# Kernel tuning notes

Measured on AMD Instinct MI355X. Metric: run time of the kernel, lower is better.

The kernel has to match this reference:

```python
import jax, jax.numpy as jnp
import numpy as np

LN_EPS = 1e-5


def _layer_norm(x, g, b):
    m = jnp.mean(x, axis=-1, keepdims=True)
    v = jnp.mean(jnp.square(x - m), axis=-1, keepdims=True)
    return (x - m) * jax.lax.rsqrt(v + LN_EPS) * g + b


def _transition(x, g, bln, w_sw, w_ss, w_sig, b_sig, w_scale, residual):
    # TransitionBlock, eval mode (dropout = identity)
    x_in = x
    x = _layer_norm(x, g, bln)
    b = jax.nn.silu(x @ w_sw.T) * (x @ w_ss.T)
    y = jax.nn.sigmoid(x @ w_sig.T + b_sig) * (b @ w_scale.T)
    return x_in + y if residual else y


def setup_inputs() -> dict:
    N, E = 1000000, 100000
    F_DIM, A_DIM, H_DIM, HEADS = 64, 128, 256, 4
    D_IN = F_DIM + A_DIM
    key = jax.random.key(0)
    ks = jax.random.split(key, 16)
    s = 0.02
    inp = {
        'v_equivariant': jax.random.normal(ks[0], (N, 3), jnp.float32),
        'v_atom_features': jax.random.normal(ks[1], (N, A_DIM), jnp.float32),
        'edge_group_idx': jnp.sort(jax.random.randint(ks[2], (N,), 0, E)).astype(jnp.int32),
        'num_edges': E,
        'fourier_w': jax.random.normal(ks[3], (F_DIM,), jnp.float32),
        'fourier_b': jax.random.normal(ks[4], (F_DIM,), jnp.float32),
        # TransitionBlock 1 (input 192 -> 256, no residual)
        'tb1_ln_g': jnp.ones((D_IN,), jnp.float32),
        'tb1_ln_b': jnp.zeros((D_IN,), jnp.float32),
        'tb1_w_sw': jax.random.normal(ks[5], (H_DIM, D_IN), jnp.float32) * s,
        'tb1_w_ss': jax.random.normal(ks[6], (H_DIM, D_IN), jnp.float32) * s,
        'tb1_w_sig': jax.random.normal(ks[7], (H_DIM, D_IN), jnp.float32) * s,
        'tb1_b_sig': jnp.full((H_DIM,), -2.0, jnp.float32),
        'tb1_w_scale': jax.random.normal(ks[8], (H_DIM, H_DIM), jnp.float32) * s,
        # TransitionBlock 2 (256 -> 256, residual)
        'tb2_ln_g': jnp.ones((H_DIM,), jnp.float32),
        'tb2_ln_b': jnp.zeros((H_DIM,), jnp.float32),
        'tb2_w_sw': jax.random.normal(ks[9], (H_DIM, H_DIM), jnp.float32) * s,
        'tb2_w_ss': jax.random.normal(ks[10], (H_DIM, H_DIM), jnp.float32) * s,
        'tb2_w_sig': jax.random.normal(ks[11], (H_DIM, H_DIM), jnp.float32) * s,
        'tb2_b_sig': jnp.full((H_DIM,), -2.0, jnp.float32),
        'tb2_w_scale': jax.random.normal(ks[12], (H_DIM, H_DIM), jnp.float32) * s,
        # final linear 256 -> num_heads
        'out_w': jax.random.normal(ks[13], (HEADS, H_DIM), jnp.float32) * s,
        'out_b': jnp.zeros((HEADS,), jnp.float32),
    }
    return inp


def reference(v_equivariant, v_atom_features, edge_group_idx, num_edges,
              fourier_w, fourier_b,
              tb1_ln_g, tb1_ln_b, tb1_w_sw, tb1_w_ss, tb1_w_sig, tb1_b_sig, tb1_w_scale,
              tb2_ln_g, tb2_ln_b, tb2_w_sw, tb2_w_ss, tb2_w_sig, tb2_b_sig, tb2_w_scale,
              out_w, out_b):
    # Fourier embedding of vector norms: [N] -> [N, F_DIM]
    v_norms = jnp.linalg.norm(v_equivariant, axis=-1)
    f_dist = jnp.cos(2.0 * jnp.pi * (v_norms[..., None] * fourier_w + fourier_b))
    x = jnp.concatenate([f_dist, v_atom_features], axis=-1)  # [N, 192]
    x = _transition(x, tb1_ln_g, tb1_ln_b, tb1_w_sw, tb1_w_ss, tb1_w_sig, tb1_b_sig, tb1_w_scale, residual=False)
    x = _transition(x, tb2_ln_g, tb2_ln_b, tb2_w_sw, tb2_w_ss, tb2_w_sig, tb2_b_sig, tb2_w_scale, residual=True)
    scores = x @ out_w.T + out_b  # [N, H]
    # scatter_softmax over edge groups (per head)
    smax = jax.ops.segment_max(scores, edge_group_idx, num_segments=num_edges)
    e = jnp.exp(scores - smax[edge_group_idx])
    ssum = jax.ops.segment_sum(e, edge_group_idx, num_segments=num_edges)
    alphas = e / ssum[edge_group_idx]  # [N, H]
    # weighted scatter-sum pooling of 3-vectors per head
    v_weighted = v_equivariant[:, None, :] * alphas[..., None]  # [N, H, 3]
    v_pooled = jax.ops.segment_sum(v_weighted, edge_group_idx, num_segments=num_edges)
    return v_pooled.reshape(num_edges, -1)  # [E, H*3]
```

## Files before the change

kernel.cpp:

```cpp
#include <hip/hip_runtime.h>
#include <math.h>

#define DIN   192
#define HD    256
#define ROWS  64
#define THREADS 256
#define LSTR  256

typedef __bf16 bf16_t;
typedef bf16_t bf16x8 __attribute__((ext_vector_type(8)));
typedef unsigned short u16x8 __attribute__((ext_vector_type(8)));
typedef float  f32x16 __attribute__((ext_vector_type(16)));

static __device__ __forceinline__ f32x16 mfma32(bf16x8 a, bf16x8 b, f32x16 c) {
  return __builtin_amdgcn_mfma_f32_32x32x16_bf16(a, b, c, 0, 0, 0);
}
static __device__ __forceinline__ unsigned short f2bfu(float f) {
  bf16_t h = (bf16_t)f; unsigned short u; __builtin_memcpy(&u, &h, 2); return u;
}
static __device__ __forceinline__ float bfu2f(unsigned short u) {
  unsigned x = ((unsigned)u) << 16; float f; __builtin_memcpy(&f, &x, 4); return f;
}
static __device__ __forceinline__ unsigned pk2(float a, float b) {
  return (unsigned)f2bfu(a) | ((unsigned)f2bfu(b) << 16);
}
static __device__ __forceinline__ float lo16(unsigned u) { return bfu2f((unsigned short)(u & 0xffff)); }
static __device__ __forceinline__ float hi16(unsigned u) { return bfu2f((unsigned short)(u >> 16)); }
static __device__ __forceinline__ float sigm(float x) {
  return __builtin_amdgcn_rcpf(1.f + __expf(-x));
}
static __device__ __forceinline__ int lidx(int row, int col) {
  return row * LSTR + (col ^ ((row & 7) << 3));
}
static __device__ __forceinline__ int crow(int r, int kg) {
  return (r & 3) + 8 * (r >> 2) + 4 * kg;
}

#define OFF_WSW1 0
#define OFF_WSS1 49152
#define OFF_WSG1 98304
#define OFF_WSC1 147456
#define OFF_WSW2 212992
#define OFF_WSS2 278528
#define OFF_WSG2 344064
#define OFF_WSC2 409600
#define OFF_WOUT 475136
#define NGRP_REORD 59392
#define NGRP_ALL   60416

__global__ void iab_wconv_kernel(const float* __restrict__ a0, const float* __restrict__ a1,
                                 const float* __restrict__ a2, const float* __restrict__ a3,
                                 const float* __restrict__ a4, const float* __restrict__ a5,
                                 const float* __restrict__ a6, const float* __restrict__ a7,
                                 const float* __restrict__ a8, unsigned short* __restrict__ out)
{
  const int i = blockIdx.x * 256 + threadIdx.x;
  if (i >= NGRP_ALL) return;
  if (i >= NGRP_REORD) {
    const int g  = i - NGRP_REORD;
    const int ks = g >> 6;
    const int ln = g & 63;
    const int col = ln & 31;
    const int kg  = ln >> 5;
    #pragma unroll
    for (int j = 0; j < 8; ++j) {
      const float vv = (col < 4) ? a8[col * 256 + ks * 16 + kg * 8 + j] : 0.f;
      out[OFF_WOUT + (size_t)g * 8 + j] = f2bfu(vv);
    }
    return;
  }
  const float* src; int off, Kd, g;
  if      (i < 6144)  { src = a0; off = OFF_WSW1; Kd = 192; g = i; }
  else if (i < 12288) { src = a1; off = OFF_WSS1; Kd = 192; g = i - 6144; }
  else if (i < 18432) { src = a2; off = OFF_WSG1; Kd = 192; g = i - 12288; }
  else if (i < 26624) { src = a3; off = OFF_WSC1; Kd = 256; g = i - 18432; }
  else if (i < 34816) { src = a4; off = OFF_WSW2; Kd = 256; g = i - 26624; }
  else if (i < 43008) { src = a5; off = OFF_WSS2; Kd = 256; g = i - 34816; }
  else if (i < 51200) { src = a6; off = OFF_WSG2; Kd = 256; g = i - 43008; }
  else                { src = a7; off = OFF_WSC2; Kd = 256; g = i - 51200; }
  const int KS   = Kd >> 4;
  const int tile = g / (KS * 64);
  const int rem  = g - tile * (KS * 64);
  const int ks   = rem >> 6;
  const int ln   = rem & 63;
  const float* sp = src + (size_t)(tile * 32 + (ln & 31)) * Kd + ks * 16 + (ln >> 5) * 8;
  #pragma unroll
  for (int j = 0; j < 8; ++j) out[off + (size_t)g * 8 + j] = f2bfu(sp[j]);
}

template<int KS>
static __device__ __forceinline__ void bphase2(const unsigned short* __restrict__ Wsw,
                                               const unsigned short* __restrict__ Wss,
                                               const unsigned short* __restrict__ sIn,
                                               unsigned short* __restrict__ sOut,
                                               int l31, int kg, int xr, int ocol)
{
  f32x16 u0{}, u1{}, s0{}, s1{};
  #pragma unroll 2
  for (int ks = 0; ks < KS; ++ks) {
    const bf16x8 wa = *(const bf16x8*)(Wsw + ks * 512);
    const bf16x8 wb = *(const bf16x8*)(Wss + ks * 512);
    const int off = ((ks * 16) + kg * 8) ^ xr;
    const bf16x8 A0 = *(const bf16x8*)(sIn + l31 * LSTR + off);
    const bf16x8 A1 = *(const bf16x8*)(sIn + (32 + l31) * LSTR + off);
    u0 = mfma32(A0, wa, u0); u1 = mfma32(A1, wa, u1);
    s0 = mfma32(A0, wb, s0); s1 = mfma32(A1, wb, s1);
  }
  #pragma unroll
  for (int i = 0; i < 16; ++i) {
    const float x0 = u0[i];
    const float x1 = u1[i];
    sOut[lidx(crow(i, kg),      ocol)] = f2bfu(x0 * sigm(x0) * s0[i]);
    sOut[lidx(32 + crow(i, kg), ocol)] = f2bfu(x1 * sigm(x1) * s1[i]);
  }
}

template<int KSG, int RES>
static __device__ __forceinline__ void cphase2(const unsigned short* __restrict__ Wg,
                                               const unsigned short* __restrict__ Wc,
                                               const unsigned short* __restrict__ sAin,
                                               const unsigned short* __restrict__ sBin,
                                               int l31, int kg, int xr, float bias,
                                               unsigned (&x0)[8], unsigned (&x1)[8])
{
  unsigned pg0[8], pg1[8];
  {
    f32x16 g0{}, g1{};
    #pragma unroll 4
    for (int ks = 0; ks < KSG; ++ks) {
      const bf16x8 wg = *(const bf16x8*)(Wg + ks * 512);
      const int off = ((ks * 16) + kg * 8) ^ xr;
      const bf16x8 A0 = *(const bf16x8*)(sAin + l31 * LSTR + off);
      const bf16x8 A1 = *(const bf16x8*)(sAin + (32 + l31) * LSTR + off);
      g0 = mfma32(A0, wg, g0);
      g1 = mfma32(A1, wg, g1);
    }
    #pragma unroll
    for (int p = 0; p < 8; ++p) {
      pg0[p] = pk2(sigm(g0[2*p] + bias), sigm(g0[2*p+1] + bias));
      pg1[p] = pk2(sigm(g1[2*p] + bias), sigm(g1[2*p+1] + bias));
    }
  }
  {
    f32x16 c0{}, c1{};
    #pragma unroll 4
    for (int ks = 0; ks < 16; ++ks) {
      const bf16x8 wv = *(const bf16x8*)(Wc + ks * 512);
      const int off = ((ks * 16) + kg * 8) ^ xr;
      const bf16x8 A0 = *(const bf16x8*)(sBin + l31 * LSTR + off);
      const bf16x8 A1 = *(const bf16x8*)(sBin + (32 + l31) * LSTR + off);
      c0 = mfma32(A0, wv, c0);
      c1 = mfma32(A1, wv, c1);
    }
    #pragma unroll
    for (int p = 0; p < 8; ++p) {
      const float ya0 = lo16(pg0[p]) * c0[2*p],  ya1 = hi16(pg0[p]) * c0[2*p+1];
      const float yb0 = lo16(pg1[p]) * c1[2*p],  yb1 = hi16(pg1[p]) * c1[2*p+1];
      if (RES) {
        x0[p] = pk2(lo16(x0[p]) + ya0, hi16(x0[p]) + ya1);
        x1[p] = pk2(lo16(x1[p]) + yb0, hi16(x1[p]) + yb1);
      } else {
        x0[p] = pk2(ya0, ya1);
        x1[p] = pk2(yb0, yb1);
      }
    }
  }
}

static __device__ __forceinline__ void storePk2(unsigned short* dst,
                                                const unsigned (&x0)[8], const unsigned (&x1)[8],
                                                int kg, int ocol)
{
  #pragma unroll
  for (int p = 0; p < 8; ++p) {
    const int r0 = crow(2 * p, kg);
    dst[lidx(r0,          ocol)] = (unsigned short)(x0[p] & 0xffff);
    dst[lidx(r0 + 1,      ocol)] = (unsigned short)(x0[p] >> 16);
    dst[lidx(32 + r0,     ocol)] = (unsigned short)(x1[p] & 0xffff);
    dst[lidx(32 + r0 + 1, ocol)] = (unsigned short)(x1[p] >> 16);
  }
}

#define LNACC(P) { \
  float e_; \
  e_ = bfu2f(P[0]); s += e_; sq += e_ * e_; \
  e_ = bfu2f(P[1]); s += e_; sq += e_ * e_; \
  e_ = bfu2f(P[2]); s += e_; sq += e_ * e_; \
  e_ = bfu2f(P[3]); s += e_; sq += e_ * e_; \
  e_ = bfu2f(P[4]); s += e_; sq += e_ * e_; \
  e_ = bfu2f(P[5]); s += e_; sq += e_ * e_; \
  e_ = bfu2f(P[6]); s += e_; sq += e_ * e_; \
  e_ = bfu2f(P[7]); s += e_; sq += e_ * e_; }

#define LNNORM(P, GPTR, BPTR, BASE) { \
  const int base_ = (BASE); \
  const float4 ga_ = *(const float4*)((GPTR) + base_); \
  const float4 gb_ = *(const float4*)((GPTR) + base_ + 4); \
  const float4 oa_ = *(const float4*)((BPTR) + base_); \
  const float4 ob_ = *(const float4*)((BPTR) + base_ + 4); \
  u16x8 q_; \
  q_[0] = f2bfu((bfu2f(P[0]) - mean) * rstd * ga_.x + oa_.x); \
  q_[1] = f2bfu((bfu2f(P[1]) - mean) * rstd * ga_.y + oa_.y); \
  q_[2] = f2bfu((bfu2f(P[2]) - mean) * rstd * ga_.z + oa_.z); \
  q_[3] = f2bfu((bfu2f(P[3]) - mean) * rstd * ga_.w + oa_.w); \
  q_[4] = f2bfu((bfu2f(P[4]) - mean) * rstd * gb_.x + ob_.x); \
  q_[5] = f2bfu((bfu2f(P[5]) - mean) * rstd * gb_.y + ob_.y); \
  q_[6] = f2bfu((bfu2f(P[6]) - mean) * rstd * gb_.z + ob_.z); \
  q_[7] = f2bfu((bfu2f(P[7]) - mean) * rstd * gb_.w + ob_.w); \
  *(u16x8*)(sA + r * LSTR + (base_ ^ xrr)) = q_; }

__global__ __launch_bounds__(THREADS, 2)
void iab_rows_mfma(
    const float* __restrict__ v, const float* __restrict__ af,
    const float* __restrict__ fw, const float* __restrict__ fb,
    const float* __restrict__ ln1g, const float* __restrict__ ln1b,
    const float* __restrict__ bsig1,
    const float* __restrict__ ln2g, const float* __restrict__ ln2b,
    const float* __restrict__ bsig2,
    const float* __restrict__ outb,
    const unsigned short* __restrict__ wc,
    float* __restrict__ scores, int N)
{
  __shared__ __align__(16) unsigned short sA[ROWS * LSTR];
  __shared__ __align__(16) unsigned short sB[ROWS * LSTR];

  const int t    = threadIdx.x;
  const int w    = t >> 6;
  const int lane = t & 63;
  const int l31  = lane & 31;
  const int kg   = lane >> 5;
  const int xr   = (lane & 7) << 3;
  const int row0 = blockIdx.x * ROWS;
  const int oc0  = w * 64 + l31;
  const int oc1  = oc0 + 32;
  const int T0   = w * 2;
  const int T1   = w * 2 + 1;
  const int lb   = lane * 8;

  #pragma unroll 1
  for (int it = 0; it < 2; ++it) {
    const int r   = (t >> 3) + it * 32;
    const int sub = t & 7;
    const int g   = row0 + r;
    const int xrr = (r & 7) << 3;
    float s = 0.f, sq = 0.f;
    u16x8 p0, p1 = {}, p2 = {};
    {
      float vx = 0.f, vy = 0.f, vz = 0.f;
      if (g < N) {
        vx = v[3 * (size_t)g + 0];
        vy = v[3 * (size_t)g + 1];
        vz = v[3 * (size_t)g + 2];
      }
      const float nrm = sqrtf(vx * vx + vy * vy + vz * vz);
      const float4 fwa = *(const float4*)(fw + sub * 8);
      const float4 fwb = *(const float4*)(fw + sub * 8 + 4);
      const float4 fba = *(const float4*)(fb + sub * 8);
      const float4 fbb = *(const float4*)(fb + sub * 8 + 4);
      const float e0 = __cosf(6.283185307179586f * (nrm * fwa.x + fba.x));
      const float e1 = __cosf(6.283185307179586f * (nrm * fwa.y + fba.y));
      const float e2 = __cosf(6.283185307179586f * (nrm * fwa.z + fba.z));
      const float e3 = __cosf(6.283185307179586f * (nrm * fwa.w + fba.w));
      const float e4 = __cosf(6.283185307179586f * (nrm * fwb.x + fbb.x));
      const float e5 = __cosf(6.283185307179586f * (nrm * fwb.y + fbb.y));
      const float e6 = __cosf(6.283185307179586f * (nrm * fwb.z + fbb.z));
      const float e7 = __cosf(6.283185307179586f * (nrm * fwb.w + fbb.w));
      s  += e0 + e1 + e2 + e3 + e4 + e5 + e6 + e7;
      sq += e0*e0 + e1*e1 + e2*e2 + e3*e3 + e4*e4 + e5*e5 + e6*e6 + e7*e7;
      p0[0] = f2bfu(e0); p0[1] = f2bfu(e1); p0[2] = f2bfu(e2); p0[3] = f2bfu(e3);
      p0[4] = f2bfu(e4); p0[5] = f2bfu(e5); p0[6] = f2bfu(e6); p0[7] = f2bfu(e7);
    }
    if (g < N) {
      const float* ap = af + (size_t)g * 128 + sub * 8;
      {
        const float4 a0 = *(const float4*)(ap);
        const float4 a1 = *(const float4*)(ap + 4);
        s  += a0.x + a0.y + a0.z + a0.w + a1.x + a1.y + a1.z + a1.w;
        sq += a0.x*a0.x + a0.y*a0.y + a0.z*a0.z + a0.w*a0.w
            + a1.x*a1.x + a1.y*a1.y + a1.z*a1.z + a1.w*a1.w;
        p1[0] = f2bfu(a0.x); p1[1] = f2bfu(a0.y); p1[2] = f2bfu(a0.z); p1[3] = f2bfu(a0.w);
        p1[4] = f2bfu(a1.x); p1[5] = f2bfu(a1.y); p1[6] = f2bfu(a1.z); p1[7] = f2bfu(a1.w);
      }
      {
        const float4 a2 = *(const float4*)(ap + 64);
        const float4 a3 = *(const float4*)(ap + 68);
        s  += a2.x + a2.y + a2.z + a2.w + a3.x + a3.y + a3.z + a3.w;
        sq += a2.x*a2.x + a2.y*a2.y + a2.z*a2.z + a2.w*a2.w
            + a3.x*a3.x + a3.y*a3.y + a3.z*a3.z + a3.w*a3.w;
        p2[0] = f2bfu(a2.x); p2[1] = f2bfu(a2.y); p2[2] = f2bfu(a2.z); p2[3] = f2bfu(a2.w);
        p2[4] = f2bfu(a3.x); p2[5] = f2bfu(a3.y); p2[6] = f2bfu(a3.z); p2[7] = f2bfu(a3.w);
      }
    }
    #pragma unroll
    for (int o = 1; o < 8; o <<= 1) {
      s  += __shfl_xor(s,  o);
      sq += __shfl_xor(sq, o);
    }
    const float mean = s * (1.f / 192.f);
    const float var  = fmaxf(sq * (1.f / 192.f) - mean * mean, 0.f);
    const float rstd = rsqrtf(var + 1e-5f);
    LNNORM(p0, ln1g, ln1b, sub * 8);
    LNNORM(p1, ln1g, ln1b, 64 + sub * 8);
    LNNORM(p2, ln1g, ln1b, 128 + sub * 8);
  }
  __syncthreads();

  unsigned xT0M0[8], xT0M1[8], xT1M0[8], xT1M1[8];

  bphase2<12>(wc + OFF_WSW1 + T0 * 12 * 512 + lb,
              wc + OFF_WSS1 + T0 * 12 * 512 + lb, sA, sB, l31, kg, xr, oc0);
  __builtin_amdgcn_sched_barrier(0);
  bphase2<12>(wc + OFF_WSW1 + T1 * 12 * 512 + lb,
              wc + OFF_WSS1 + T1 * 12 * 512 + lb, sA, sB, l31, kg, xr, oc1);
  __syncthreads();

  cphase2<12, 0>(wc + OFF_WSG1 + T0 * 12 * 512 + lb,
                 wc + OFF_WSC1 + T0 * 16 * 512 + lb,
                 sA, sB, l31, kg, xr, bsig1[oc0], xT0M0, xT0M1);
  __builtin_amdgcn_sched_barrier(0);
  cphase2<12, 0>(wc + OFF_WSG1 + T1 * 12 * 512 + lb,
                 wc + OFF_WSC1 + T1 * 16 * 512 + lb,
                 sA, sB, l31, kg, xr, bsig1[oc1], xT1M0, xT1M1);
  __syncthreads();

  storePk2(sA, xT0M0, xT0M1, kg, oc0);
  storePk2(sA, xT1M0, xT1M1, kg, oc1);
  __syncthreads();

  #pragma unroll 1
  for (int it = 0; it < 2; ++it) {
    const int r   = (t >> 3) + it * 32;
    const int sub = t & 7;
    const int xrr = (r & 7) << 3;
    const u16x8 rv0 = *(const u16x8*)(sA + r * LSTR + ((sub * 32 +  0) ^ xrr));
    const u16x8 rv1 = *(const u16x8*)(sA + r * LSTR + ((sub * 32 +  8) ^ xrr));
    const u16x8 rv2 = *(const u16x8*)(sA + r * LSTR + ((sub * 32 + 16) ^ xrr));
    const u16x8 rv3 = *(const u16x8*)(sA + r * LSTR + ((sub * 32 + 24) ^ xrr));
    float s = 0.f, sq = 0.f;
    LNACC(rv0);
    LNACC(rv1);
    LNACC(rv2);
    LNACC(rv3);
    #pragma unroll
    for (int o = 1; o < 8; o <<= 1) {
      s  += __shfl_xor(s,  o);
      sq += __shfl_xor(sq, o);
    }
    const float mean = s * (1.f / 256.f);
    const float var  = fmaxf(sq * (1.f / 256.f) - mean * mean, 0.f);
    const float rstd = rsqrtf(var + 1e-5f);
    LNNORM(rv0, ln2g, ln2b, sub * 32 +  0);
    LNNORM(rv1, ln2g, ln2b, sub * 32 +  8);
    LNNORM(rv2, ln2g, ln2b, sub * 32 + 16);
    LNNORM(rv3, ln2g, ln2b, sub * 32 + 24);
  }
  __syncthreads();

  bphase2<16>(wc + OFF_WSW2 + T0 * 16 * 512 + lb,
              wc + OFF_WSS2 + T0 * 16 * 512 + lb, sA, sB, l31, kg, xr, oc0);
  __builtin_amdgcn_sched_barrier(0);
  bphase2<16>(wc + OFF_WSW2 + T1 * 16 * 512 + lb,
              wc + OFF_WSS2 + T1 * 16 * 512 + lb, sA, sB, l31, kg, xr, oc1);
  __syncthreads();

  cphase2<16, 1>(wc + OFF_WSG2 + T0 * 16 * 512 + lb,
                 wc + OFF_WSC2 + T0 * 16 * 512 + lb,
                 sA, sB, l31, kg, xr, bsig2[oc0], xT0M0, xT0M1);
  __builtin_amdgcn_sched_barrier(0);
  cphase2<16, 1>(wc + OFF_WSG2 + T1 * 16 * 512 + lb,
                 wc + OFF_WSC2 + T1 * 16 * 512 + lb,
                 sA, sB, l31, kg, xr, bsig2[oc1], xT1M0, xT1M1);
  __syncthreads();

  storePk2(sA, xT0M0, xT0M1, kg, oc0);
  storePk2(sA, xT1M0, xT1M1, kg, oc1);
  __syncthreads();

  if (w < 2) {
    const unsigned short* WtF = wc + OFF_WOUT + (size_t)lane * 8;
    f32x16 c{};
    #pragma unroll 4
    for (int ks = 0; ks < 16; ++ks) {
      const bf16x8 wf = *(const bf16x8*)(WtF + ks * 512);
      const bf16x8 A  = *(const bf16x8*)(sA + (w * 32 + l31) * LSTR + (((ks * 16) + kg * 8) ^ xr));
      c = mfma32(A, wf, c);
    }
    if (l31 < 4) {
      const float bias = outb[l31];
      #pragma unroll
      for (int i = 0; i < 16; ++i) {
        const int g = row0 + w * 32 + crow(i, kg);
        if (g < N) scores[(size_t)g * 4 + l31] = c[i] + bias;
      }
    }
  }
}

__device__ __forceinline__ int iab_lower_bound(const int* __restrict__ a, int n, int key)
{
  int lo = 0, hi = n;
  while (lo < hi) {
    const int mid = (lo + hi) >> 1;
    if (a[mid] < key) lo = mid + 1; else hi = mid;
  }
  return lo;
}

__global__ __launch_bounds__(256)
void iab_segpool_kernel(const float* __restrict__ scores,
                        const float* __restrict__ v,
                        const int* __restrict__ gidx,
                        float* __restrict__ out, int N, int E)
{
  const int seg  = blockIdx.x * 4 + (threadIdx.x >> 6);
  const int lane = threadIdx.x & 63;
  if (seg >= E) return;

  const int lo = iab_lower_bound(gidx, N, seg);
  const int hi = iab_lower_bound(gidx, N, seg + 1);

  const int h  = lane & 3;
  const int ro = lane >> 2;

  float m = -INFINITY;
  for (int base = lo; base < hi; base += 16) {
    const int r = base + ro;
    if (r < hi) m = fmaxf(m, scores[(size_t)r * 4 + h]);
  }
  #pragma unroll
  for (int o = 4; o < 64; o <<= 1) m = fmaxf(m, __shfl_xor(m, o));

  float ssum = 0.f, w0 = 0.f, w1 = 0.f, w2 = 0.f;
  for (int base = lo; base < hi; base += 16) {
    const int r = base + ro;
    if (r < hi) {
      const float e = expf(scores[(size_t)r * 4 + h] - m);
      ssum += e;
      w0 += e * v[3 * (size_t)r + 0];
      w1 += e * v[3 * (size_t)r + 1];
      w2 += e * v[3 * (size_t)r + 2];
    }
  }
  #pragma unroll
  for (int o = 4; o < 64; o <<= 1) {
    ssum += __shfl_xor(ssum, o);
    w0   += __shfl_xor(w0, o);
    w1   += __shfl_xor(w1, o);
    w2   += __shfl_xor(w2, o);
  }

  if (ro == 0) {
    const float inv = (hi > lo) ? (1.f / ssum) : 0.f;
    out[(size_t)seg * 12 + h * 3 + 0] = w0 * inv;
    out[(size_t)seg * 12 + h * 3 + 1] = w1 * inv;
    out[(size_t)seg * 12 + h * 3 + 2] = w2 * inv;
  }
}

extern "C" void kernel_launch(void* const* d_in, const int* in_sizes, int n_in,
                              void* d_out, int out_size, void* d_ws, size_t ws_size,
                              hipStream_t stream)
{
  const float* v     = (const float*)d_in[0];
  const float* af    = (const float*)d_in[1];
  const int*   gidx  = (const int*)  d_in[2];
  const float* fw    = (const float*)d_in[4];
  const float* fb    = (const float*)d_in[5];
  const float* ln1g  = (const float*)d_in[6];
  const float* ln1b  = (const float*)d_in[7];
  const float* wsw1  = (const float*)d_in[8];
  const float* wss1  = (const float*)d_in[9];
  const float* wsig1 = (const float*)d_in[10];
  const float* bsig1 = (const float*)d_in[11];
  const float* wsc1  = (const float*)d_in[12];
  const float* ln2g  = (const float*)d_in[13];
  const float* ln2b  = (const float*)d_in[14];
  const float* wsw2  = (const float*)d_in[15];
  const float* wss2  = (const float*)d_in[16];
  const float* wsig2 = (const float*)d_in[17];
  const float* bsig2 = (const float*)d_in[18];
  const float* wsc2  = (const float*)d_in[19];
  const float* outw  = (const float*)d_in[20];
  const float* outb  = (const float*)d_in[21];

  const int N = in_sizes[0] / 3;
  const int E = out_size / 12;

  float* scores = (float*)d_ws;
  unsigned short* wcv = (unsigned short*)((char*)d_ws + (size_t)N * 4 * sizeof(float));

  hipLaunchKernelGGL(iab_wconv_kernel, dim3((NGRP_ALL + 255) / 256), dim3(256), 0, stream,
                     wsw1, wss1, wsig1, wsc1, wsw2, wss2, wsig2, wsc2, outw, wcv);

  hipLaunchKernelGGL(iab_rows_mfma, dim3((N + ROWS - 1) / ROWS), dim3(THREADS), 0, stream,
                     v, af, fw, fb, ln1g, ln1b, bsig1, ln2g, ln2b, bsig2, outb,
                     wcv, scores, N);

  hipLaunchKernelGGL(iab_segpool_kernel, dim3((E + 3) / 4), dim3(256), 0, stream,
                     scores, v, gidx, (float*)d_out, N, E);
}
```

Baseline: 2.080 ms.

## Switch row kernel to 16x16x32 MFMA with 32-row tiles and higher occupancy

Result: slower. 2.433 ms (+17.0%).

```diff
diff --git a/kernel.cpp b/kernel.cpp
--- a/kernel.cpp
+++ b/kernel.cpp
@@ -3,17 +3,17 @@
 
 #define DIN   192
 #define HD    256
-#define ROWS  64
+#define ROWS  32
 #define THREADS 256
 #define LSTR  256
 
 typedef __bf16 bf16_t;
 typedef bf16_t bf16x8 __attribute__((ext_vector_type(8)));
 typedef unsigned short u16x8 __attribute__((ext_vector_type(8)));
-typedef float  f32x16 __attribute__((ext_vector_type(16)));
-
-static __device__ __forceinline__ f32x16 mfma32(bf16x8 a, bf16x8 b, f32x16 c) {
-  return __builtin_amdgcn_mfma_f32_32x32x16_bf16(a, b, c, 0, 0, 0);
+typedef float  f32x4  __attribute__((ext_vector_type(4)));
+
+static __device__ __forceinline__ f32x4 mfma16(bf16x8 a, bf16x8 b, f32x4 c) {
+  return __builtin_amdgcn_mfma_f32_16x16x32_bf16(a, b, c, 0, 0, 0);
 }
 static __device__ __forceinline__ unsigned short f2bfu(float f) {
   bf16_t h = (bf16_t)f; unsigned short u; __builtin_memcpy(&u, &h, 2); return u;
@@ -31,9 +31,6 @@
 }
 static __device__ __forceinline__ int lidx(int row, int col) {
   return row * LSTR + (col ^ ((row & 7) << 3));
-}
-static __device__ __forceinline__ int crow(int r, int kg) {
-  return (r & 3) + 8 * (r >> 2) + 4 * kg;
 }
 
 #define OFF_WSW1 0
@@ -46,7 +43,7 @@
 #define OFF_WSC2 409600
 #define OFF_WOUT 475136
 #define NGRP_REORD 59392
-#define NGRP_ALL   60416
+#define NGRP_ALL   59904
 
 __global__ void iab_wconv_kernel(const float* __restrict__ a0, const float* __restrict__ a1,
                                  const float* __restrict__ a2, const float* __restrict__ a3,
@@ -60,11 +57,11 @@
     const int g  = i - NGRP_REORD;
     const int ks = g >> 6;
     const int ln = g & 63;
-    const int col = ln & 31;
-    const int kg  = ln >> 5;
+    const int col = ln & 15;
+    const int g4  = ln >> 4;
     #pragma unroll
     for (int j = 0; j < 8; ++j) {
-      const float vv = (col < 4) ? a8[col * 256 + ks * 16 + kg * 8 + j] : 0.f;
+      const float vv = (col < 4) ? a8[col * 256 + ks * 32 + g4 * 8 + j] : 0.f;
       out[OFF_WOUT + (size_t)g * 8 + j] = f2bfu(vv);
     }
     return;
@@ -78,106 +75,105 @@
   else if (i < 43008) { src = a5; off = OFF_WSS2; Kd = 256; g = i - 34816; }
   else if (i < 51200) { src = a6; off = OFF_WSG2; Kd = 256; g = i - 43008; }
   else                { src = a7; off = OFF_WSC2; Kd = 256; g = i - 51200; }
-  const int KS   = Kd >> 4;
-  const int tile = g / (KS * 64);
-  const int rem  = g - tile * (KS * 64);
+  const int KS32 = Kd >> 5;
+  const int tile = g / (KS32 * 64);
+  const int rem  = g - tile * (KS32 * 64);
   const int ks   = rem >> 6;
   const int ln   = rem & 63;
-  const float* sp = src + (size_t)(tile * 32 + (ln & 31)) * Kd + ks * 16 + (ln >> 5) * 8;
+  const float* sp = src + (size_t)(tile * 16 + (ln & 15)) * Kd + ks * 32 + (ln >> 4) * 8;
   #pragma unroll
   for (int j = 0; j < 8; ++j) out[off + (size_t)g * 8 + j] = f2bfu(sp[j]);
 }
 
-template<int KS>
-static __device__ __forceinline__ void bphase2(const unsigned short* __restrict__ Wsw,
-                                               const unsigned short* __restrict__ Wss,
-                                               const unsigned short* __restrict__ sIn,
-                                               unsigned short* __restrict__ sOut,
-                                               int l31, int kg, int xr, int ocol)
-{
-  f32x16 u0{}, u1{}, s0{}, s1{};
+template<int KS32>
+static __device__ __forceinline__ void bphase16(const unsigned short* __restrict__ Wsw,
+                                                const unsigned short* __restrict__ Wss,
+                                                const unsigned short* __restrict__ sIn,
+                                                unsigned short* __restrict__ sOut,
+                                                int cc, int kb, int xr, int g4, int ocol)
+{
+  f32x4 u0{}, u1{}, s0{}, s1{};
   #pragma unroll 2
-  for (int ks = 0; ks < KS; ++ks) {
+  for (int ks = 0; ks < KS32; ++ks) {
     const bf16x8 wa = *(const bf16x8*)(Wsw + ks * 512);
     const bf16x8 wb = *(const bf16x8*)(Wss + ks * 512);
-    const int off = ((ks * 16) + kg * 8) ^ xr;
-    const bf16x8 A0 = *(const bf16x8*)(sIn + l31 * LSTR + off);
-    const bf16x8 A1 = *(const bf16x8*)(sIn + (32 + l31) * LSTR + off);
-    u0 = mfma32(A0, wa, u0); u1 = mfma32(A1, wa, u1);
-    s0 = mfma32(A0, wb, s0); s1 = mfma32(A1, wb, s1);
-  }
-  #pragma unroll
-  for (int i = 0; i < 16; ++i) {
-    const float x0 = u0[i];
-    const float x1 = u1[i];
-    sOut[lidx(crow(i, kg),      ocol)] = f2bfu(x0 * sigm(x0) * s0[i]);
-    sOut[lidx(32 + crow(i, kg), ocol)] = f2bfu(x1 * sigm(x1) * s1[i]);
-  }
-}
-
-template<int KSG, int RES>
-static __device__ __forceinline__ void cphase2(const unsigned short* __restrict__ Wg,
-                                               const unsigned short* __restrict__ Wc,
-                                               const unsigned short* __restrict__ sAin,
-                                               const unsigned short* __restrict__ sBin,
-                                               int l31, int kg, int xr, float bias,
-                                               unsigned (&x0)[8], unsigned (&x1)[8])
-{
-  unsigned pg0[8], pg1[8];
+    const int off = (ks * 32 + kb) ^ xr;
+    const bf16x8 A0 = *(const bf16x8*)(sIn + cc * LSTR + off);
+    const bf16x8 A1 = *(const bf16x8*)(sIn + (16 + cc) * LSTR + off);
+    u0 = mfma16(A0, wa, u0); u1 = mfma16(A1, wa, u1);
+    s0 = mfma16(A0, wb, s0); s1 = mfma16(A1, wb, s1);
+  }
+  #pragma unroll
+  for (int r = 0; r < 4; ++r) {
+    const float x0 = u0[r];
+    const float x1 = u1[r];
+    sOut[lidx(g4 * 4 + r,      ocol)] = f2bfu(x0 * sigm(x0) * s0[r]);
+    sOut[lidx(16 + g4 * 4 + r, ocol)] = f2bfu(x1 * sigm(x1) * s1[r]);
+  }
+}
+
+template<int KSG32, int RES>
+static __device__ __forceinline__ void cphase16(const unsigned short* __restrict__ Wg,
+                                                const unsigned short* __restrict__ Wc,
+                                                const unsigned short* __restrict__ sAin,
+                                                const unsigned short* __restrict__ sBin,
+                                                int cc, int kb, int xr, float bias,
+                                                unsigned (&x)[4])
+{
+  unsigned pg[4];
   {
-    f32x16 g0{}, g1{};
+    f32x4 g0{}, g1{};
     #pragma unroll 4
-    for (int ks = 0; ks < KSG; ++ks) {
+    for (int ks = 0; ks < KSG32; ++ks) {
       const bf16x8 wg = *(const bf16x8*)(Wg + ks * 512);
-      const int off = ((ks * 16) + kg * 8) ^ xr;
-      const bf16x8 A0 = *(const bf16x8*)(sAin + l31 * LSTR + off);
-      const bf16x8 A1 = *(const bf16x8*)(sAin + (32 + l31) * LSTR + off);
-      g0 = mfma32(A0, wg, g0);
-      g1 = mfma32(A1, wg, g1);
-    }
+      const int off = (ks * 32 + kb) ^ xr;
+      const bf16x8 A0 = *(const bf16x8*)(sAin + cc * LSTR + off);
+      const bf16x8 A1 = *(const bf16x8*)(sAin + (16 + cc) * LSTR + off);
+      g0 = mfma16(A0, wg, g0);
+      g1 = mfma16(A1, wg, g1);
+    }
+    pg[0] = pk2(sigm(g0[0] + bias), sigm(g0[1] + bias));
+    pg[1] = pk2(sigm(g0[2] + bias), sigm(g0[3] + bias));
+    pg[2] = pk2(sigm(g1[0] + bias), sigm(g1[1] + bias));
+    pg[3] = pk2(sigm(g1[2] + bias), sigm(g1[3] + bias));
+  }
+  {
+    f32x4 c0{}, c1{};
+    #pragma unroll 4
+    for (int ks = 0; ks < 8; ++ks) {
+      const bf16x8 wv = *(const bf16x8*)(Wc + ks * 512);
+      const int off = (ks * 32 + kb) ^ xr;
+      const bf16x8 A0 = *(const bf16x8*)(sBin + cc * LSTR + off);
+      const bf16x8 A1 = *(const bf16x8*)(sBin + (16 + cc) * LSTR + off);
+      c0 = mfma16(A0, wv, c0);
+      c1 = mfma16(A1, wv, c1);
+    }
+    if (RES) {
+      x[0] = pk2(lo16(x[0]) + lo16(pg[0]) * c0[0], hi16(x[0]) + hi16(pg[0]) * c0[1]);
+      x[1] = pk2(lo16(x[1]) + lo16(pg[1]) * c0[2], hi16(x[1]) + hi16(pg[1]) * c0[3]);
+      x[2] = pk2(lo16(x[2]) + lo16(pg[2]) * c1[0], hi16(x[2]) + hi16(pg[2]) * c1[1]);
+      x[3] = pk2(lo16(x[3]) + lo16(pg[3]) * c1[2], hi16(x[3]) + hi16(pg[3]) * c1[3]);
+    } else {
+      x[0] = pk2(lo16(pg[0]) * c0[0], hi16(pg[0]) * c0[1]);
+      x[1] = pk2(lo16(pg[1]) * c0[2], hi16(pg[1]) * c0[3]);
+      x[2] = pk2(lo16(pg[2]) * c1[0], hi16(pg[2]) * c1[1]);
+      x[3] = pk2(lo16(pg[3]) * c1[2], hi16(pg[3]) * c1[3]);
+    }
+  }
+}
+
+static __device__ __forceinline__ void storePk16(unsigned short* dst, const unsigned (&x)[4],
+                                                 int g4, int ocol)
+{
+  #pragma unroll
+  for (int m = 0; m < 2; ++m) {
     #pragma unroll
-    for (int p = 0; p < 8; ++p) {
-      pg0[p] = pk2(sigm(g0[2*p] + bias), sigm(g0[2*p+1] + bias));
-      pg1[p] = pk2(sigm(g1[2*p] + bias), sigm(g1[2*p+1] + bias));
-    }
-  }
-  {
-    f32x16 c0{}, c1{};
-    #pragma unroll 4
-    for (int ks = 0; ks < 16; ++ks) {
-      const bf16x8 wv = *(const bf16x8*)(Wc + ks * 512);
-      const int off = ((ks * 16) + kg * 8) ^ xr;
-      const bf16x8 A0 = *(const bf16x8*)(sBin + l31 * LSTR + off);
-      const bf16x8 A1 = *(const bf16x8*)(sBin + (32 + l31) * LSTR + off);
-      c0 = mfma32(A0, wv, c0);
-      c1 = mfma32(A1, wv, c1);
-    }
-    #pragma unroll
-    for (int p = 0; p < 8; ++p) {
-      const float ya0 = lo16(pg0[p]) * c0[2*p],  ya1 = hi16(pg0[p]) * c0[2*p+1];
-      const float yb0 = lo16(pg1[p]) * c1[2*p],  yb1 = hi16(pg1[p]) * c1[2*p+1];
-      if (RES) {
-        x0[p] = pk2(lo16(x0[p]) + ya0, hi16(x0[p]) + ya1);
-        x1[p] = pk2(lo16(x1[p]) + yb0, hi16(x1[p]) + yb1);
-      } else {
-        x0[p] = pk2(ya0, ya1);
-        x1[p] = pk2(yb0, yb1);
-      }
-    }
-  }
-}
-
-static __device__ __forceinline__ void storePk2(unsigned short* dst,
-                                                const unsigned (&x0)[8], const unsigned (&x1)[8],
-                                                int kg, int ocol)
-{
-  #pragma unroll
-  for (int p = 0; p < 8; ++p) {
-    const int r0 = crow(2 * p, kg);
-    dst[lidx(r0,          ocol)] = (unsigned short)(x0[p] & 0xffff);
-    dst[lidx(r0 + 1,      ocol)] = (unsigned short)(x0[p] >> 16);
-    dst[lidx(32 + r0,     ocol)] = (unsigned short)(x1[p] & 0xffff);
-    dst[lidx(32 + r0 + 1, ocol)] = (unsigned short)(x1[p] >> 16);
+    for (int p = 0; p < 2; ++p) {
+      const unsigned pk = x[m * 2 + p];
+      const int r0 = m * 16 + g4 * 4 + 2 * p;
+      dst[lidx(r0,     ocol)] = (unsigned short)(pk & 0xffff);
+      dst[lidx(r0 + 1, ocol)] = (unsigned short)(pk >> 16);
+    }
   }
 }
 
@@ -209,7 +205,7 @@
   q_[7] = f2bfu((bfu2f(P[7]) - mean) * rstd * gb_.w + ob_.w); \
   *(u16x8*)(sA + r * LSTR + (base_ ^ xrr)) = q_; }
 
-__global__ __launch_bounds__(THREADS, 2)
+__global__ __launch_bounds__(THREADS, 4)
 void iab_rows_mfma(
     const float* __restrict__ v, const float* __restrict__ af,
     const float* __restrict__ fw, const float* __restrict__ fb,
@@ -227,19 +223,15 @@
   const int t    = threadIdx.x;
   const int w    = t >> 6;
   const int lane = t & 63;
-  const int l31  = lane & 31;
-  const int kg   = lane >> 5;
-  const int xr   = (lane & 7) << 3;
+  const int cc   = lane & 15;
+  const int g4   = lane >> 4;
+  const int kb   = g4 * 8;
+  const int xr   = (cc & 7) << 3;
   const int row0 = blockIdx.x * ROWS;
-  const int oc0  = w * 64 + l31;
-  const int oc1  = oc0 + 32;
-  const int T0   = w * 2;
-  const int T1   = w * 2 + 1;
   const int lb   = lane * 8;
 
-  #pragma unroll 1
-  for (int it = 0; it < 2; ++it) {
-    const int r   = (t >> 3) + it * 32;
+  {
+    const int r   = t >> 3;
     const int sub = t & 7;
     const int g   = row0 + r;
     const int xrr = (r & 7) << 3;
@@ -305,31 +297,34 @@
   }
   __syncthreads();
 
-  unsigned xT0M0[8], xT0M1[8], xT1M0[8], xT1M1[8];
-
-  bphase2<12>(wc + OFF_WSW1 + T0 * 12 * 512 + lb,
-              wc + OFF_WSS1 + T0 * 12 * 512 + lb, sA, sB, l31, kg, xr, oc0);
-  __builtin_amdgcn_sched_barrier(0);
-  bphase2<12>(wc + OFF_WSW1 + T1 * 12 * 512 + lb,
-              wc + OFF_WSS1 + T1 * 12 * 512 + lb, sA, sB, l31, kg, xr, oc1);
-  __syncthreads();
-
-  cphase2<12, 0>(wc + OFF_WSG1 + T0 * 12 * 512 + lb,
-                 wc + OFF_WSC1 + T0 * 16 * 512 + lb,
-                 sA, sB, l31, kg, xr, bsig1[oc0], xT0M0, xT0M1);
-  __builtin_amdgcn_sched_barrier(0);
-  cphase2<12, 0>(wc + OFF_WSG1 + T1 * 12 * 512 + lb,
-                 wc + OFF_WSC1 + T1 * 16 * 512 + lb,
-                 sA, sB, l31, kg, xr, bsig1[oc1], xT1M0, xT1M1);
-  __syncthreads();
-
-  storePk2(sA, xT0M0, xT0M1, kg, oc0);
-  storePk2(sA, xT1M0, xT1M1, kg, oc1);
-  __syncthreads();
+  unsigned x2[4][4];
 
   #pragma unroll 1
-  for (int it = 0; it < 2; ++it) {
-    const int r   = (t >> 3) + it * 32;
+  for (int c = 0; c < 4; ++c) {
+    const int T = w * 4 + c;
+    bphase16<6>(wc + OFF_WSW1 + T * 6 * 512 + lb,
+                wc + OFF_WSS1 + T * 6 * 512 + lb,
+                sA, sB, cc, kb, xr, g4, w * 64 + c * 16 + cc);
+  }
+  __syncthreads();
+
+  #pragma unroll
+  for (int c = 0; c < 4; ++c) {
+    const int T = w * 4 + c;
+    const int ocol = w * 64 + c * 16 + cc;
+    cphase16<6, 0>(wc + OFF_WSG1 + T * 6 * 512 + lb,
+                   wc + OFF_WSC1 + T * 8 * 512 + lb,
+                   sA, sB, cc, kb, xr, bsig1[ocol], x2[c]);
+  }
+  __syncthreads();
+
+  #pragma unroll
+  for (int c = 0; c < 4; ++c)
+    storePk16(sA, x2[c], g4, w * 64 + c * 16 + cc);
+  __syncthreads();
+
+  {
+    const int r   = t >> 3;
     const int sub = t & 7;
     const int xrr = (r & 7) << 3;
     const u16x8 rv0 = *(const u16x8*)(sA + r * LSTR + ((sub * 32 +  0) ^ xrr));
@@ -356,41 +351,45 @@
   }
   __syncthreads();
 
-  bphase2<16>(wc + OFF_WSW2 + T0 * 16 * 512 + lb,
-              wc + OFF_WSS2 + T0 * 16 * 512 + lb, sA, sB, l31, kg, xr, oc0);
-  __builtin_amdgcn_sched_barrier(0);
-  bphase2<16>(wc + OFF_WSW2 + T1 * 16 * 512 + lb,
-              wc + OFF_WSS2 + T1 * 16 * 512 + lb, sA, sB, l31, kg, xr, oc1);
-  __syncthreads();
-
-  cphase2<16, 1>(wc + OFF_WSG2 + T0 * 16 * 512 + lb,
-                 wc + OFF_WSC2 + T0 * 16 * 512 + lb,
-                 sA, sB, l31, kg, xr, bsig2[oc0], xT0M0, xT0M1);
-  __builtin_amdgcn_sched_barrier(0);
-  cphase2<16, 1>(wc + OFF_WSG2 + T1 * 16 * 512 + lb,
-                 wc + OFF_WSC2 + T1 * 16 * 512 + lb,
-                 sA, sB, l31, kg, xr, bsig2[oc1], xT1M0, xT1M1);
-  __syncthreads();
-
-  storePk2(sA, xT0M0, xT0M1, kg, oc0);
-  storePk2(sA, xT1M0, xT1M1, kg, oc1);
+  #pragma unroll 1
+  for (int c = 0; c < 4; ++c) {
+    const int T = w * 4 + c;
+    bphase16<8>(wc + OFF_WSW2 + T * 8 * 512 + lb,
+                wc + OFF_WSS2 + T * 8 * 512 + lb,
+                sA, sB, cc, kb, xr, g4, w * 64 + c * 16 + cc);
+  }
+  __syncthreads();
+
+  #pragma unroll
+  for (int c = 0; c < 4; ++c) {
+    const int T = w * 4 + c;
+    const int ocol = w * 64 + c * 16 + cc;
+    cphase16<8, 1>(wc + OFF_WSG2 + T * 8 * 512 + lb,
+                   wc + OFF_WSC2 + T * 8 * 512 + lb,
+                   sA, sB, cc, kb, xr, bsig2[ocol], x2[c]);
+  }
+  __syncthreads();
+
+  #pragma unroll
+  for (int c = 0; c < 4; ++c)
+    storePk16(sA, x2[c], g4, w * 64 + c * 16 + cc);
   __syncthreads();
 
   if (w < 2) {
     const unsigned short* WtF = wc + OFF_WOUT + (size_t)lane * 8;
-    f32x16 c{};
+    f32x4 c{};
     #pragma unroll 4
-    for (int ks = 0; ks < 16; ++ks) {
+    for (int ks = 0; ks < 8; ++ks) {
       const bf16x8 wf = *(const bf16x8*)(WtF + ks * 512);
-      const bf16x8 A  = *(const bf16x8*)(sA + (w * 32 + l31) * LSTR + (((ks * 16) + kg * 8) ^ xr));
-      c = mfma32(A, wf, c);
-    }
-    if (l31 < 4) {
-      const float bias = outb[l31];
+      const bf16x8 A  = *(const bf16x8*)(sA + (w * 16 + cc) * LSTR + ((ks * 32 + kb) ^ xr));
+      c = mfma16(A, wf, c);
+    }
+    if (cc < 4) {
+      const float bias = outb[cc];
       #pragma unroll
-      for (int i = 0; i < 16; ++i) {
-        const int g = row0 + w * 32 + crow(i, kg);
-        if (g < N) scores[(size_t)g * 4 + l31] = c[i] + bias;
+      for (int r = 0; r < 4; ++r) {
+        const int g = row0 + w * 16 + g4 * 4 + r;
+        if (g < N) scores[(size_t)g * 4 + cc] = c[r] + bias;
       }
     }
   }
```
